# Kernel optimization log

Measured on AMD Instinct MI355X. Metric: run time of the kernel, lower is better.

## Reference

```python
import jax, jax.numpy as jnp
import numpy as np

HEADS = 4
DIM_HEADS = 32


def setup_inputs() -> dict:
    key = jax.random.key(0)
    ks = jax.random.split(key, 6)
    dim = 128
    hidden = HEADS * DIM_HEADS  # 128
    b, h, w = 4, 64, 64
    s = 0.02
    return {
        "x": jax.random.normal(ks[0], (b, dim, h, w), dtype=jnp.float32),
        "wq": jax.random.normal(ks[1], (hidden, dim), dtype=jnp.float32) * s,
        "wk": jax.random.normal(ks[2], (hidden, dim), dtype=jnp.float32) * s,
        "wv": jax.random.normal(ks[3], (hidden, dim), dtype=jnp.float32) * s,
        "wo": jax.random.normal(ks[4], (dim, hidden), dtype=jnp.float32) * s,
        "bo": jnp.zeros((dim,), dtype=jnp.float32),
    }


def reference(x, wq, wk, wv, wo, bo):
    b, c, h, w = x.shape
    n = h * w
    scale = DIM_HEADS ** (-0.5)
    xt = x.reshape(b, c, n)  # [b, c, n]; 1x1 conv == matmul over channel dim
    # project and split heads: [b, heads, dim_heads, n]
    q = jnp.einsum('oc,bcn->bon', wq, xt).reshape(b, HEADS, DIM_HEADS, n)
    k = jnp.einsum('oc,bcn->bon', wk, xt).reshape(b, HEADS, DIM_HEADS, n)
    v = jnp.einsum('oc,bcn->bon', wv, xt).reshape(b, HEADS, DIM_HEADS, n)
    q = q * scale
    sim = jnp.einsum('bhdi,bhdj->bhij', q, k)  # [b, heads, n, n]
    attn = jax.nn.softmax(sim, axis=-1)
    out = jnp.einsum('bhij,bhdj->bhid', attn, v)  # [b, heads, n, dim_heads]
    # permute to [b, heads, dim_heads, n] then merge heads -> channels
    out = out.transpose(0, 1, 3, 2).reshape(b, HEADS * DIM_HEADS, n)
    out = jnp.einsum('oc,bcn->bon', wo, out) + bo[None, :, None]
    return out.reshape(b, -1, h, w)
```

## Files before the change

### kernel.cpp

```cpp
#include <hip/hip_runtime.h>
#include <cstdint>

typedef __bf16 bf16;
typedef __bf16 bf16x2 __attribute__((ext_vector_type(2)));
typedef __bf16 bf16x4 __attribute__((ext_vector_type(4)));
typedef __bf16 bf16x8 __attribute__((ext_vector_type(8)));
typedef float f32x4 __attribute__((ext_vector_type(4)));
typedef float f32x16 __attribute__((ext_vector_type(16)));

#define MFMA16(a, b, c) __builtin_amdgcn_mfma_f32_16x16x32_bf16(a, b, c, 0, 0, 0)
#define MFMA32(a, b, c) __builtin_amdgcn_mfma_f32_32x32x16_bf16(a, b, c, 0, 0, 0)

static constexpr int N = 4096;
static constexpr int CDIM = 128;
static constexpr int NH = 4;
static constexpr int DH = 32;

__device__ __forceinline__ uint32_t pack_bf16_trunc(float a, float b) {
    return __builtin_amdgcn_perm(__builtin_bit_cast(uint32_t, b),
                                 __builtin_bit_cast(uint32_t, a), 0x07060302u);
}

__device__ __forceinline__ bf16 to_bf16_rnd(float f) {
    uint32_t u = __builtin_bit_cast(uint32_t, f);
    return __builtin_bit_cast(bf16, (uint16_t)((u + 0x8000u) >> 16));
}

__global__ __launch_bounds__(256) void cvt_w(const float* __restrict__ wq,
                                             const float* __restrict__ wk,
                                             const float* __restrict__ wv,
                                             const float* __restrict__ wo,
                                             bf16* __restrict__ W) {
    int i = blockIdx.x * 256 + threadIdx.x;
    const float qs = 0.17677669529663687f * 1.4426950408889634f;
    W[i]         = (bf16)(wq[i] * qs);
    W[16384 + i] = to_bf16_rnd(wk[i]);
    W[32768 + i] = to_bf16_rnd(wv[i]);
    W[49152 + i] = to_bf16_rnd(wo[i]);
}

__global__ __launch_bounds__(256) void proj_qkv(const float* __restrict__ x,
                                                const bf16* __restrict__ W,
                                                bf16* __restrict__ Q,
                                                bf16* __restrict__ K,
                                                bf16* __restrict__ V) {
    const int b = blockIdx.y;
    const int wt = blockIdx.z;
    const int n0 = blockIdx.x * 64;
    __shared__ __align__(16) bf16 xT[64][136];
    const int tid = threadIdx.x;
    const float* xb = x + (size_t)b * CDIM * N;
    for (int i = tid; i < 64 * 128; i += 256) {
        int n = i & 63, cc = i >> 6;
        xT[n][cc] = to_bf16_rnd(xb[(size_t)cc * N + n0 + n]);
    }
    __syncthreads();

    const int lane = tid & 63, w = tid >> 6;
    const int cr = lane & 15, quad = lane >> 4;

    const bf16* Wm = W + wt * 16384;
    for (int nt = 0; nt < 4; ++nt) {
        bf16x8 bfr[4];
#pragma unroll
        for (int ks = 0; ks < 4; ++ks)
            bfr[ks] = *(const bf16x8*)&xT[nt * 16 + cr][ks * 32 + quad * 8];
#pragma unroll
        for (int ot2 = 0; ot2 < 2; ++ot2) {
            int ot = w * 2 + ot2;
            f32x4 acc = {0.f, 0.f, 0.f, 0.f};
#pragma unroll
            for (int ks = 0; ks < 4; ++ks) {
                bf16x8 afr = *(const bf16x8*)&Wm[(ot * 16 + cr) * 128 + ks * 32 + quad * 8];
                acc = MFMA16(afr, bfr[ks], acc);
            }
            int n = n0 + nt * 16 + cr;
            int o0 = ot * 16 + quad * 4;
            if (wt < 2) {
                bf16* dst = (wt == 0) ? Q : K;
                int h = o0 >> 5, d0 = o0 & 31;
                bf16* p = dst + (((size_t)(b * NH + h) * N + n) * DH + d0);
                *(bf16x2*)p       = (bf16x2){(bf16)acc[0], (bf16)acc[1]};
                *(bf16x2*)(p + 2) = (bf16x2){(bf16)acc[2], (bf16)acc[3]};
            } else {
                int h = o0 >> 5, d0 = o0 & 31;
                int k6 = nt * 16 + cr;
                int r4 = (k6 >> 2) & 3;
                int slotgrp = ((r4 & 1) << 1) | (r4 >> 1);
                int kperm = (k6 & ~15) | (slotgrp * 4 + (k6 & 3));
                bf16* p = V + ((size_t)(b * NH + h) * 64 + blockIdx.x) * 2048 + kperm;
#pragma unroll
                for (int r = 0; r < 4; ++r)
                    p[(d0 + r) * 64] = (bf16)acc[r];
            }
        }
    }
}

__global__ __launch_bounds__(256, 2) void flash(const bf16* __restrict__ Q,
                                                const bf16* __restrict__ K,
                                                const bf16* __restrict__ V,
                                                bf16* __restrict__ O) {
    const int gid = blockIdx.x;
    const int bh = gid & 15;
    const int tid = threadIdx.x;
    const int w = tid >> 6, lane = tid & 63;
    const int l31 = lane & 31, h = lane >> 5;
    const int q0w = (gid >> 4) * 128 + w * 32;

    __shared__ __align__(16) bf16 Kl[2][64 * 40];
    __shared__ __align__(16) bf16 Vl[2][32 * 72];

    const bf16* Qb = Q + (size_t)bh * N * DH;
    const bf16* Kb = K + (size_t)bh * N * DH;
    const bf16* Vt = V + (size_t)bh * 64 * 2048;

    const int k_dst = (tid >> 2) * 40 + (tid & 3) * 8;
    const int v_dst = (tid >> 3) * 72 + (tid & 7) * 8;

    const bf16x8 qf0 = *(const bf16x8*)&Qb[(q0w + l31) * DH + h * 8];
    const bf16x8 qf1 = *(const bf16x8*)&Qb[(q0w + l31) * DH + 16 + h * 8];

    bf16x8 ones;
#pragma unroll
    for (int i = 0; i < 8; ++i) ones[i] = (bf16)1.0f;

    f32x16 out = {};
    f32x16 accL = {};

    {
        bf16x8 kreg = *(const bf16x8*)(Kb + tid * 8);
        bf16x8 vreg = *(const bf16x8*)(Vt + tid * 8);
        *(bf16x8*)&Kl[0][k_dst] = kreg;
        *(bf16x8*)&Vl[0][v_dst] = vreg;
    }
    __syncthreads();

    for (int kt = 0; kt < 64; ++kt) {
        const int cb = kt & 1;
        bf16x8 kreg, vreg;
        if (kt < 63) {
            kreg = *(const bf16x8*)(Kb + (kt + 1) * 2048 + tid * 8);
            vreg = *(const bf16x8*)(Vt + (kt + 1) * 2048 + tid * 8);
        }
        const bf16* Kc = &Kl[cb][0];
        const bf16* Vc = &Vl[cb][0];

#pragma unroll
        for (int g2 = 0; g2 < 2; ++g2) {
            bf16x8 kf0 = *(const bf16x8*)&Kc[(g2 * 32 + l31) * 40 + h * 8];
            bf16x8 kf1 = *(const bf16x8*)&Kc[(g2 * 32 + l31) * 40 + 16 + h * 8];
            f32x16 sc = {};
            sc = MFMA32(kf0, qf0, sc);
            sc = MFMA32(kf1, qf1, sc);

            uint32_t c0 = pack_bf16_trunc(__builtin_amdgcn_exp2f(sc[0]),
                                          __builtin_amdgcn_exp2f(sc[1]));
            uint32_t c1 = pack_bf16_trunc(__builtin_amdgcn_exp2f(sc[2]),
                                          __builtin_amdgcn_exp2f(sc[3]));
            uint32_t c2 = pack_bf16_trunc(__builtin_amdgcn_exp2f(sc[4]),
                                          __builtin_amdgcn_exp2f(sc[5]));
            uint32_t c3 = pack_bf16_trunc(__builtin_amdgcn_exp2f(sc[6]),
                                          __builtin_amdgcn_exp2f(sc[7]));
            uint32_t c4 = pack_bf16_trunc(__builtin_amdgcn_exp2f(sc[8]),
                                          __builtin_amdgcn_exp2f(sc[9]));
            uint32_t c5 = pack_bf16_trunc(__builtin_amdgcn_exp2f(sc[10]),
                                          __builtin_amdgcn_exp2f(sc[11]));
            uint32_t c6 = pack_bf16_trunc(__builtin_amdgcn_exp2f(sc[12]),
                                          __builtin_amdgcn_exp2f(sc[13]));
            uint32_t c7 = pack_bf16_trunc(__builtin_amdgcn_exp2f(sc[14]),
                                          __builtin_amdgcn_exp2f(sc[15]));

            bf16x8 pB0, pB1;
            {
                uint32_t t0[4] = {c0, c1, c2, c3};
                uint32_t t1[4] = {c4, c5, c6, c7};
                pB0 = *(bf16x8*)t0;
                pB1 = *(bf16x8*)t1;
            }

            bf16x8 av0 = *(const bf16x8*)&Vc[l31 * 72 + g2 * 32 + h * 8];
            bf16x8 av1 = *(const bf16x8*)&Vc[l31 * 72 + g2 * 32 + 16 + h * 8];
            out = MFMA32(av0, pB0, out);
            out = MFMA32(av1, pB1, out);
            accL = MFMA32(ones, pB0, accL);
            accL = MFMA32(ones, pB1, accL);
        }

        if (kt < 63) {
            *(bf16x8*)&Kl[1 - cb][k_dst] = kreg;
            *(bf16x8*)&Vl[1 - cb][v_dst] = vreg;
        }
        __syncthreads();
    }

    const float inv = __builtin_amdgcn_rcpf(accL[0]);
    const int b = bh >> 2, hh = bh & 3;
    bf16* Ob = O + ((size_t)b * N + q0w + l31) * CDIM + hh * DH;
#pragma unroll
    for (int rg = 0; rg < 4; ++rg) {
        const int d0 = rg * 8 + h * 4;
        bf16x4 v = {(bf16)(out[rg * 4 + 0] * inv), (bf16)(out[rg * 4 + 1] * inv),
                    (bf16)(out[rg * 4 + 2] * inv), (bf16)(out[rg * 4 + 3] * inv)};
        *(bf16x4*)(Ob + d0) = v;
    }
}

__global__ __launch_bounds__(256) void proj_o(const bf16* __restrict__ A,
                                              const bf16* __restrict__ W,
                                              const float* __restrict__ bo,
                                              float* __restrict__ out) {
    const int b = blockIdx.y;
    const int n0 = blockIdx.x * 64;
    __shared__ __align__(16) bf16 aT[64][136];
    const int tid = threadIdx.x;
    const bf16* Ab = A + (size_t)b * N * CDIM;
    for (int i = tid; i < 64 * 64; i += 256) {
        int c2 = i & 63, n = i >> 6;
        *(uint32_t*)&aT[n][c2 * 2] = *(const uint32_t*)&Ab[(size_t)(n0 + n) * CDIM + c2 * 2];
    }
    __syncthreads();

    const int lane = tid & 63, w = tid >> 6;
    const int cr = lane & 15, quad = lane >> 4;
    const bf16* Wm = W + 3 * 16384;
    const int ot = blockIdx.z * 4 + w;

    for (int nt = 0; nt < 4; ++nt) {
        bf16x8 bfr[4];
#pragma unroll
        for (int ks = 0; ks < 4; ++ks)
            bfr[ks] = *(const bf16x8*)&aT[nt * 16 + cr][ks * 32 + quad * 8];
        f32x4 acc = {0.f, 0.f, 0.f, 0.f};
#pragma unroll
        for (int ks = 0; ks < 4; ++ks) {
            bf16x8 afr = *(const bf16x8*)&Wm[(ot * 16 + cr) * 128 + ks * 32 + quad * 8];
            acc = MFMA16(afr, bfr[ks], acc);
        }
        int n = n0 + nt * 16 + cr;
        int o0 = ot * 16 + quad * 4;
#pragma unroll
        for (int r = 0; r < 4; ++r)
            out[((size_t)b * CDIM + o0 + r) * N + n] = acc[r] + bo[o0 + r];
    }
}

extern "C" void kernel_launch(void* const* d_in, const int* in_sizes, int n_in,
                              void* d_out, int out_size, void* d_ws, size_t ws_size,
                              hipStream_t stream) {
    const float* x  = (const float*)d_in[0];
    const float* wq = (const float*)d_in[1];
    const float* wk = (const float*)d_in[2];
    const float* wv = (const float*)d_in[3];
    const float* wo = (const float*)d_in[4];
    const float* bo = (const float*)d_in[5];

    char* ws = (char*)d_ws;
    bf16* Q = (bf16*)(ws);
    bf16* K = (bf16*)(ws + ((size_t)4 << 20));
    bf16* V = (bf16*)(ws + ((size_t)8 << 20));
    bf16* A = (bf16*)(ws + ((size_t)12 << 20));
    bf16* W = (bf16*)(ws + ((size_t)16 << 20));

    cvt_w<<<64, 256, 0, stream>>>(wq, wk, wv, wo, W);
    proj_qkv<<<dim3(64, 4, 3), 256, 0, stream>>>(x, W, Q, K, V);
    flash<<<512, 256, 0, stream>>>(Q, K, V, A);
    proj_o<<<dim3(64, 4, 2), 256, 0, stream>>>(A, W, bo, (float*)d_out);
}
```

Baseline: 136.4 us.

## Split keys across warp pairs in flash, reuse K/V over two query tiles, widen loads

The flash kernel now gives each warp two 32-row query tiles and splits the key range between warp pairs. Each loaded K/V fragment is reused for twice as many queries, and the loop runs half as many iterations with twice the shared-memory staging. The two key halves' partial outputs and row sums are combined through shared memory at the end. The projection kernels also switch to wider vector loads (float4 and bf16x8). The cost is more registers and shared memory per block, which may lower occupancy, plus an extra reduction step and sync.

```diff
diff --git a/kernel.cpp b/kernel.cpp
--- a/kernel.cpp
+++ b/kernel.cpp
@@ -50,9 +50,13 @@
     __shared__ __align__(16) bf16 xT[64][136];
     const int tid = threadIdx.x;
     const float* xb = x + (size_t)b * CDIM * N;
-    for (int i = tid; i < 64 * 128; i += 256) {
-        int n = i & 63, cc = i >> 6;
-        xT[n][cc] = to_bf16_rnd(xb[(size_t)cc * N + n0 + n]);
+    for (int i = tid; i < 64 * 32; i += 256) {
+        int n4 = (i & 15) * 4, cc = i >> 4;
+        const float4 v = *(const float4*)&xb[(size_t)cc * N + n0 + n4];
+        xT[n4 + 0][cc] = to_bf16_rnd(v.x);
+        xT[n4 + 1][cc] = to_bf16_rnd(v.y);
+        xT[n4 + 2][cc] = to_bf16_rnd(v.z);
+        xT[n4 + 3][cc] = to_bf16_rnd(v.w);
     }
     __syncthreads();
 
@@ -103,106 +107,146 @@
                                                 bf16* __restrict__ O) {
     const int gid = blockIdx.x;
     const int bh = gid & 15;
+    const int qblk = gid >> 4;
     const int tid = threadIdx.x;
     const int w = tid >> 6, lane = tid & 63;
     const int l31 = lane & 31, h = lane >> 5;
-    const int q0w = (gid >> 4) * 128 + w * 32;
-
-    __shared__ __align__(16) bf16 Kl[2][64 * 40];
-    __shared__ __align__(16) bf16 Vl[2][32 * 72];
+    const int qg = w >> 1, kh = w & 1;
+    const int qbase = qblk * 128 + qg * 64;
+
+    __shared__ __align__(16) bf16 Kl[2][2][64 * 40];
+    __shared__ __align__(16) bf16 Vl[2][2][32 * 72];
 
     const bf16* Qb = Q + (size_t)bh * N * DH;
     const bf16* Kb = K + (size_t)bh * N * DH;
     const bf16* Vt = V + (size_t)bh * 64 * 2048;
 
+    const bf16* ksrc0 = Kb + tid * 8;
+    const bf16* ksrc1 = Kb + 65536 + tid * 8;
+    const bf16* vsrc0 = Vt + tid * 8;
+    const bf16* vsrc1 = Vt + 65536 + tid * 8;
     const int k_dst = (tid >> 2) * 40 + (tid & 3) * 8;
     const int v_dst = (tid >> 3) * 72 + (tid & 7) * 8;
 
-    const bf16x8 qf0 = *(const bf16x8*)&Qb[(q0w + l31) * DH + h * 8];
-    const bf16x8 qf1 = *(const bf16x8*)&Qb[(q0w + l31) * DH + 16 + h * 8];
+    bf16x8 qf[2][2];
+#pragma unroll
+    for (int qs = 0; qs < 2; ++qs)
+#pragma unroll
+        for (int dh = 0; dh < 2; ++dh)
+            qf[qs][dh] = *(const bf16x8*)&Qb[(qbase + qs * 32 + l31) * DH + dh * 16 + h * 8];
 
     bf16x8 ones;
 #pragma unroll
     for (int i = 0; i < 8; ++i) ones[i] = (bf16)1.0f;
 
-    f32x16 out = {};
-    f32x16 accL = {};
-
-    {
-        bf16x8 kreg = *(const bf16x8*)(Kb + tid * 8);
-        bf16x8 vreg = *(const bf16x8*)(Vt + tid * 8);
-        *(bf16x8*)&Kl[0][k_dst] = kreg;
-        *(bf16x8*)&Vl[0][v_dst] = vreg;
-    }
+    f32x16 out[2] = {};
+    f32x16 accL[2] = {};
+
+    *(bf16x8*)&Kl[0][0][k_dst] = *(const bf16x8*)ksrc0;
+    *(bf16x8*)&Kl[0][1][k_dst] = *(const bf16x8*)ksrc1;
+    *(bf16x8*)&Vl[0][0][v_dst] = *(const bf16x8*)vsrc0;
+    *(bf16x8*)&Vl[0][1][v_dst] = *(const bf16x8*)vsrc1;
     __syncthreads();
 
-    for (int kt = 0; kt < 64; ++kt) {
+    for (int kt = 0; kt < 32; ++kt) {
         const int cb = kt & 1;
-        bf16x8 kreg, vreg;
-        if (kt < 63) {
-            kreg = *(const bf16x8*)(Kb + (kt + 1) * 2048 + tid * 8);
-            vreg = *(const bf16x8*)(Vt + (kt + 1) * 2048 + tid * 8);
-        }
-        const bf16* Kc = &Kl[cb][0];
-        const bf16* Vc = &Vl[cb][0];
+        bf16x8 pk0, pk1, pv0, pv1;
+        if (kt < 31) {
+            pk0 = *(const bf16x8*)(ksrc0 + (kt + 1) * 2048);
+            pk1 = *(const bf16x8*)(ksrc1 + (kt + 1) * 2048);
+            pv0 = *(const bf16x8*)(vsrc0 + (kt + 1) * 2048);
+            pv1 = *(const bf16x8*)(vsrc1 + (kt + 1) * 2048);
+        }
+        const bf16* Kc = &Kl[cb][kh][0];
+        const bf16* Vc = &Vl[cb][kh][0];
 
 #pragma unroll
         for (int g2 = 0; g2 < 2; ++g2) {
             bf16x8 kf0 = *(const bf16x8*)&Kc[(g2 * 32 + l31) * 40 + h * 8];
             bf16x8 kf1 = *(const bf16x8*)&Kc[(g2 * 32 + l31) * 40 + 16 + h * 8];
-            f32x16 sc = {};
-            sc = MFMA32(kf0, qf0, sc);
-            sc = MFMA32(kf1, qf1, sc);
-
-            uint32_t c0 = pack_bf16_trunc(__builtin_amdgcn_exp2f(sc[0]),
-                                          __builtin_amdgcn_exp2f(sc[1]));
-            uint32_t c1 = pack_bf16_trunc(__builtin_amdgcn_exp2f(sc[2]),
-                                          __builtin_amdgcn_exp2f(sc[3]));
-            uint32_t c2 = pack_bf16_trunc(__builtin_amdgcn_exp2f(sc[4]),
-                                          __builtin_amdgcn_exp2f(sc[5]));
-            uint32_t c3 = pack_bf16_trunc(__builtin_amdgcn_exp2f(sc[6]),
-                                          __builtin_amdgcn_exp2f(sc[7]));
-            uint32_t c4 = pack_bf16_trunc(__builtin_amdgcn_exp2f(sc[8]),
-                                          __builtin_amdgcn_exp2f(sc[9]));
-            uint32_t c5 = pack_bf16_trunc(__builtin_amdgcn_exp2f(sc[10]),
-                                          __builtin_amdgcn_exp2f(sc[11]));
-            uint32_t c6 = pack_bf16_trunc(__builtin_amdgcn_exp2f(sc[12]),
-                                          __builtin_amdgcn_exp2f(sc[13]));
-            uint32_t c7 = pack_bf16_trunc(__builtin_amdgcn_exp2f(sc[14]),
-                                          __builtin_amdgcn_exp2f(sc[15]));
-
-            bf16x8 pB0, pB1;
-            {
-                uint32_t t0[4] = {c0, c1, c2, c3};
-                uint32_t t1[4] = {c4, c5, c6, c7};
-                pB0 = *(bf16x8*)t0;
-                pB1 = *(bf16x8*)t1;
-            }
-
             bf16x8 av0 = *(const bf16x8*)&Vc[l31 * 72 + g2 * 32 + h * 8];
             bf16x8 av1 = *(const bf16x8*)&Vc[l31 * 72 + g2 * 32 + 16 + h * 8];
-            out = MFMA32(av0, pB0, out);
-            out = MFMA32(av1, pB1, out);
-            accL = MFMA32(ones, pB0, accL);
-            accL = MFMA32(ones, pB1, accL);
-        }
-
-        if (kt < 63) {
-            *(bf16x8*)&Kl[1 - cb][k_dst] = kreg;
-            *(bf16x8*)&Vl[1 - cb][v_dst] = vreg;
+#pragma unroll
+            for (int qs = 0; qs < 2; ++qs) {
+                f32x16 sc = {};
+                sc = MFMA32(kf0, qf[qs][0], sc);
+                sc = MFMA32(kf1, qf[qs][1], sc);
+
+                uint32_t c0 = pack_bf16_trunc(__builtin_amdgcn_exp2f(sc[0]),
+                                              __builtin_amdgcn_exp2f(sc[1]));
+                uint32_t c1 = pack_bf16_trunc(__builtin_amdgcn_exp2f(sc[2]),
+                                              __builtin_amdgcn_exp2f(sc[3]));
+                uint32_t c2 = pack_bf16_trunc(__builtin_amdgcn_exp2f(sc[4]),
+                                              __builtin_amdgcn_exp2f(sc[5]));
+                uint32_t c3 = pack_bf16_trunc(__builtin_amdgcn_exp2f(sc[6]),
+                                              __builtin_amdgcn_exp2f(sc[7]));
+                uint32_t c4 = pack_bf16_trunc(__builtin_amdgcn_exp2f(sc[8]),
+                                              __builtin_amdgcn_exp2f(sc[9]));
+                uint32_t c5 = pack_bf16_trunc(__builtin_amdgcn_exp2f(sc[10]),
+                                              __builtin_amdgcn_exp2f(sc[11]));
+                uint32_t c6 = pack_bf16_trunc(__builtin_amdgcn_exp2f(sc[12]),
+                                              __builtin_amdgcn_exp2f(sc[13]));
+                uint32_t c7 = pack_bf16_trunc(__builtin_amdgcn_exp2f(sc[14]),
+                                              __builtin_amdgcn_exp2f(sc[15]));
+
+                bf16x8 pB0, pB1;
+                {
+                    uint32_t t0[4] = {c0, c1, c2, c3};
+                    uint32_t t1[4] = {c4, c5, c6, c7};
+                    pB0 = *(bf16x8*)t0;
+                    pB1 = *(bf16x8*)t1;
+                }
+
+                out[qs]  = MFMA32(av0, pB0, out[qs]);
+                out[qs]  = MFMA32(av1, pB1, out[qs]);
+                accL[qs] = MFMA32(ones, pB0, accL[qs]);
+                accL[qs] = MFMA32(ones, pB1, accL[qs]);
+            }
+        }
+
+        if (kt < 31) {
+            *(bf16x8*)&Kl[1 - cb][0][k_dst] = pk0;
+            *(bf16x8*)&Kl[1 - cb][1][k_dst] = pk1;
+            *(bf16x8*)&Vl[1 - cb][0][v_dst] = pv0;
+            *(bf16x8*)&Vl[1 - cb][1][v_dst] = pv1;
         }
         __syncthreads();
     }
 
-    const float inv = __builtin_amdgcn_rcpf(accL[0]);
-    const int b = bh >> 2, hh = bh & 3;
-    bf16* Ob = O + ((size_t)b * N + q0w + l31) * CDIM + hh * DH;
-#pragma unroll
-    for (int rg = 0; rg < 4; ++rg) {
-        const int d0 = rg * 8 + h * 4;
-        bf16x4 v = {(bf16)(out[rg * 4 + 0] * inv), (bf16)(out[rg * 4 + 1] * inv),
-                    (bf16)(out[rg * 4 + 2] * inv), (bf16)(out[rg * 4 + 3] * inv)};
-        *(bf16x4*)(Ob + d0) = v;
+    float* red = (float*)&Kl[0][0][0];
+    if (kh == 1) {
+#pragma unroll
+        for (int qs = 0; qs < 2; ++qs) {
+            float* r = red + ((size_t)((qg * 2 + qs) * 64 + lane)) * 20;
+            f32x4 t0 = {out[qs][0], out[qs][1], out[qs][2], out[qs][3]};
+            f32x4 t1 = {out[qs][4], out[qs][5], out[qs][6], out[qs][7]};
+            f32x4 t2 = {out[qs][8], out[qs][9], out[qs][10], out[qs][11]};
+            f32x4 t3 = {out[qs][12], out[qs][13], out[qs][14], out[qs][15]};
+            *(f32x4*)(r + 0)  = t0;
+            *(f32x4*)(r + 4)  = t1;
+            *(f32x4*)(r + 8)  = t2;
+            *(f32x4*)(r + 12) = t3;
+            r[16] = accL[qs][0];
+        }
+    }
+    __syncthreads();
+    if (kh == 0) {
+        const int b = bh >> 2, hh = bh & 3;
+#pragma unroll
+        for (int qs = 0; qs < 2; ++qs) {
+            const float* r = red + ((size_t)((qg * 2 + qs) * 64 + lane)) * 20;
+#pragma unroll
+            for (int i = 0; i < 16; ++i) out[qs][i] += r[i];
+            float inv = __builtin_amdgcn_rcpf(accL[qs][0] + r[16]);
+            bf16* Ob = O + ((size_t)b * N + qbase + qs * 32 + l31) * CDIM + hh * DH;
+#pragma unroll
+            for (int rg = 0; rg < 4; ++rg) {
+                const int d0 = rg * 8 + h * 4;
+                bf16x4 v = {(bf16)(out[qs][rg * 4 + 0] * inv), (bf16)(out[qs][rg * 4 + 1] * inv),
+                            (bf16)(out[qs][rg * 4 + 2] * inv), (bf16)(out[qs][rg * 4 + 3] * inv)};
+                *(bf16x4*)(Ob + d0) = v;
+            }
+        }
     }
 }
 
@@ -215,9 +259,9 @@
     __shared__ __align__(16) bf16 aT[64][136];
     const int tid = threadIdx.x;
     const bf16* Ab = A + (size_t)b * N * CDIM;
-    for (int i = tid; i < 64 * 64; i += 256) {
-        int c2 = i & 63, n = i >> 6;
-        *(uint32_t*)&aT[n][c2 * 2] = *(const uint32_t*)&Ab[(size_t)(n0 + n) * CDIM + c2 * 2];
+    for (int i = tid; i < 64 * 16; i += 256) {
+        int c8 = (i & 15) * 8, n = i >> 4;
+        *(bf16x8*)&aT[n][c8] = *(const bf16x8*)&Ab[(size_t)(n0 + n) * CDIM + c8];
     }
     __syncthreads();
 
```

Measured after the change: 132.4 us. 1.03x faster.
